# Kernel tuning notes

Hardware: AMD Instinct MI355X
Metric: run time of the kernel (lower is better)

The kernel has to match this reference:

```python
import jax, jax.numpy as jnp
import numpy as np
import math

N_QUBITS = 8
N_LAYERS = 3
BATCH = 8192
INPUT_DIM = 512


def _apply_1q(st, U, wire, batched):
    # st: (batch, 2,...,2) with N_QUBITS qubit axes; U: (2,2) or (batch,2,2)
    st = jnp.moveaxis(st, wire + 1, 1)
    sh = st.shape
    flat = st.reshape(sh[0], 2, -1)
    if batched:
        flat = jnp.einsum('bij,bjk->bik', U, flat)
    else:
        flat = jnp.einsum('ij,bjk->bik', U, flat)
    return jnp.moveaxis(flat.reshape(sh), 1, wire + 1)


def _apply_cnot(st, c, t):
    cax, tax = c + 1, t + 1
    zero = jnp.take(st, 0, axis=cax)
    one = jnp.take(st, 1, axis=cax)
    tax2 = tax - 1 if tax > cax else tax  # target axis shifts after control removed
    one = jnp.flip(one, axis=tax2)
    return jnp.stack([zero, one], axis=cax)


def _ry_batched(theta):
    # theta: (batch,) -> (batch,2,2) complex64
    c = jnp.cos(theta / 2)
    s = jnp.sin(theta / 2)
    row0 = jnp.stack([c, -s], axis=-1)
    row1 = jnp.stack([s, c], axis=-1)
    return jnp.stack([row0, row1], axis=-2).astype(jnp.complex64)


def _rot(phi, theta, omega):
    # PennyLane Rot = RZ(omega) RY(theta) RZ(phi), scalar params -> (2,2) complex64
    c = jnp.cos(theta / 2)
    s = jnp.sin(theta / 2)
    u00 = jnp.exp(-0.5j * (phi + omega)) * c
    u01 = -jnp.exp(0.5j * (phi - omega)) * s
    u10 = jnp.exp(-0.5j * (phi - omega)) * s
    u11 = jnp.exp(0.5j * (phi + omega)) * c
    return jnp.stack([jnp.stack([u00, u01]), jnp.stack([u10, u11])]).astype(jnp.complex64)


def _quantum_circuit(angles, q_weights):
    batch = angles.shape[0]
    st = jnp.zeros((batch, 2 ** N_QUBITS), jnp.complex64).at[:, 0].set(1.0)
    st = st.reshape((batch,) + (2,) * N_QUBITS)
    # AngleEmbedding with RY rotations
    for w in range(N_QUBITS):
        st = _apply_1q(st, _ry_batched(angles[:, w]), w, batched=True)
    # StronglyEntanglingLayers: Rot on each wire, then CNOT ring with range r
    for l in range(N_LAYERS):
        for w in range(N_QUBITS):
            st = _apply_1q(st, _rot(q_weights[l, w, 0], q_weights[l, w, 1], q_weights[l, w, 2]), w, batched=False)
        r = (l % (N_QUBITS - 1)) + 1
        for w in range(N_QUBITS):
            st = _apply_cnot(st, w, (w + r) % N_QUBITS)
    probs = st.real ** 2 + st.imag ** 2
    zs = []
    for w in range(N_QUBITS):
        p = jnp.moveaxis(probs, w + 1, 1).reshape(batch, 2, -1).sum(-1)
        zs.append(p[:, 0] - p[:, 1])  # <Z_w> = P(0) - P(1)
    return jnp.stack(zs, axis=-1)


def setup_inputs() -> dict:
    key = jax.random.key(0)
    k1, k2, k3 = jax.random.split(key, 3)
    x = jax.random.normal(k1, (BATCH, INPUT_DIM), dtype=jnp.float32)
    W = jax.random.normal(k2, (N_QUBITS, INPUT_DIM), dtype=jnp.float32) * (1.0 / math.sqrt(INPUT_DIM))
    b = jnp.zeros((N_QUBITS,), jnp.float32)
    scale = jnp.ones((N_QUBITS,), jnp.float32)
    bias = jnp.zeros((N_QUBITS,), jnp.float32)
    q_weights = 0.01 * jax.random.normal(k3, (N_LAYERS, N_QUBITS, 3), dtype=jnp.float32)
    return {"x": x, "W": W, "b": b, "scale": scale, "bias": bias, "q_weights": q_weights}


def reference(x, W, b, scale, bias, q_weights):
    proj = x @ W.T + b                                   # (batch, n_qubits)
    angles = jax.nn.sigmoid(proj * scale + bias) * jnp.float32(math.pi)
    return _quantum_circuit(angles, q_weights)           # (batch, n_qubits)
```

## Files before the change

### kernel.cpp

```cpp
#include <hip/hip_runtime.h>
#include <math.h>


namespace {

constexpr float PI_F = 3.14159265358979323846f;

struct Cx { float re, im; };

__device__ __forceinline__ float shfx(float v, int m) {
  return __shfl_xor(v, m, 64);
}

__device__ __forceinline__ void mix2(Cx &a, Cx &b,
    float u00r, float u00i, float u01r, float u01i,
    float u10r, float u10i, float u11r, float u11i) {
  float ar = a.re, ai = a.im, br = b.re, bi = b.im;
  a.re = u00r*ar - u00i*ai + u01r*br - u01i*bi;
  a.im = u00r*ai + u00i*ar + u01r*bi + u01i*br;
  b.re = u10r*ar - u10i*ai + u11r*br - u11i*bi;
  b.im = u10r*ai + u10i*ar + u11r*bi + u11i*br;
}

template<int W>
__device__ __forceinline__ void apply1q(Cx s[16],
    float u00r, float u00i, float u01r, float u01i,
    float u10r, float u10i, float u11r, float u11i, int lane) {
  if constexpr (W >= 4) {
    constexpr int step = 1 << (7 - W);
#pragma unroll
    for (int k = 0; k < 16; ++k)
      if (!(k & step))
        mix2(s[k], s[k + step], u00r,u00i,u01r,u01i,u10r,u10i,u11r,u11i);
  } else {
    constexpr int lm = 1 << (3 - W);
    const bool hi = (lane & lm) != 0;
    float cAr = hi ? u11r : u00r, cAi = hi ? u11i : u00i;
    float cBr = hi ? u10r : u01r, cBi = hi ? u10i : u01i;
#pragma unroll
    for (int k = 0; k < 16; ++k) {
      float tr = shfx(s[k].re, lm), ti = shfx(s[k].im, lm);
      float mr = s[k].re, mi = s[k].im;
      s[k].re = cAr*mr - cAi*mi + cBr*tr - cBi*ti;
      s[k].im = cAr*mi + cAi*mr + cBr*ti + cBi*tr;
    }
  }
}

template<int W>
__device__ __forceinline__ void ryW(Cx s[16], float ang, int lane) {
  float h = 0.5f * ang;
  float c = __cosf(h), sn = __sinf(h);
  apply1q<W>(s, c, 0.f, -sn, 0.f, sn, 0.f, c, 0.f, lane);
}

template<int L, int W>
__device__ __forceinline__ void rotW(Cx s[16], const float* __restrict__ qw, int lane) {
  float phi = qw[L*24 + W*3 + 0];
  float th  = qw[L*24 + W*3 + 1];
  float om  = qw[L*24 + W*3 + 2];
  float c  = __cosf(0.5f*th), sn = __sinf(0.5f*th);
  float a  = 0.5f*(phi + om), d = 0.5f*(phi - om);
  float ca = __cosf(a), sa = __sinf(a);
  float cd = __cosf(d), sd = __sinf(d);
  apply1q<W>(s, c*ca, -c*sa, -sn*cd, -sn*sd, sn*cd, -sn*sd, c*ca, c*sa, lane);
}

__device__ __forceinline__ void swapc(Cx &a, Cx &b) { Cx t = a; a = b; b = t; }

__device__ __forceinline__ void cswap(Cx &a, Cx &b, bool c) {
  float ar = a.re, ai = a.im;
  a.re = c ? b.re : a.re;  a.im = c ? b.im : a.im;
  b.re = c ? ar : b.re;    b.im = c ? ai : b.im;
}

template<int CW, int TW>
__device__ __forceinline__ void cnot(Cx s[16], int lane) {
  constexpr int pc = 7 - CW, pt = 7 - TW;
  if constexpr (pc >= 4 && pt >= 4) {
    constexpr int lmC = 1 << (pc - 4), lmT = 1 << (pt - 4);
    const bool ctl = (lane & lmC) != 0;
#pragma unroll
    for (int k = 0; k < 16; ++k) {
      float tr = shfx(s[k].re, lmT), ti = shfx(s[k].im, lmT);
      s[k].re = ctl ? tr : s[k].re;
      s[k].im = ctl ? ti : s[k].im;
    }
  } else if constexpr (pc >= 4) {
    constexpr int lmC = 1 << (pc - 4), step = 1 << pt;
    const bool ctl = (lane & lmC) != 0;
#pragma unroll
    for (int k = 0; k < 16; ++k)
      if (!(k & step)) cswap(s[k], s[k + step], ctl);
  } else if constexpr (pt >= 4) {
    constexpr int lmT = 1 << (pt - 4), cb = 1 << pc;
#pragma unroll
    for (int k = 0; k < 16; ++k)
      if (k & cb) {
        s[k].re = shfx(s[k].re, lmT);
        s[k].im = shfx(s[k].im, lmT);
      }
  } else {
    constexpr int cb = 1 << pc, tb = 1 << pt;
#pragma unroll
    for (int k = 0; k < 16; ++k)
      if ((k & cb) && !(k & tb)) swapc(s[k], s[k + tb]);
  }
}

template<int L>
__device__ __forceinline__ void rotLayer(Cx s[16], const float* __restrict__ qw, int lane) {
  rotW<L,0>(s, qw, lane); rotW<L,1>(s, qw, lane);
  rotW<L,2>(s, qw, lane); rotW<L,3>(s, qw, lane);
  rotW<L,4>(s, qw, lane); rotW<L,5>(s, qw, lane);
  rotW<L,6>(s, qw, lane); rotW<L,7>(s, qw, lane);
}

__global__ __launch_bounds__(256) void quantum_layer_kernel(
    const float* __restrict__ x, const float* __restrict__ Wm,
    const float* __restrict__ bvec, const float* __restrict__ scale,
    const float* __restrict__ bias, const float* __restrict__ qw,
    float* __restrict__ out) {
  const int tid  = threadIdx.x;
  const int lane = tid & 63;
  const int ll   = lane & 15;
  const int b    = blockIdx.x * 16 + (tid >> 4);

  const float4* x4 = (const float4*)(x + (size_t)b * 512);
  float4 xs[8];
#pragma unroll
  for (int j = 0; j < 8; ++j) xs[j] = x4[j * 16 + ll];
  const float4* W4 = (const float4*)Wm;
  float ang[8];
#pragma unroll
  for (int q = 0; q < 8; ++q) {
    float acc = 0.f;
#pragma unroll
    for (int j = 0; j < 8; ++j) {
      float4 w = W4[q * 128 + j * 16 + ll];
      acc += xs[j].x*w.x + xs[j].y*w.y + xs[j].z*w.z + xs[j].w*w.w;
    }
    ang[q] = acc;
  }
#pragma unroll
  for (int off = 8; off >= 1; off >>= 1)
#pragma unroll
    for (int q = 0; q < 8; ++q)
      ang[q] += shfx(ang[q], off);
#pragma unroll
  for (int q = 0; q < 8; ++q) {
    float t = (ang[q] + bvec[q]) * scale[q] + bias[q];
    ang[q] = PI_F / (1.f + __expf(-t));
  }

  Cx s[16];
#pragma unroll
  for (int k = 0; k < 16; ++k) { s[k].re = 0.f; s[k].im = 0.f; }
  s[0].re = (ll == 0) ? 1.f : 0.f;

  ryW<0>(s, ang[0], lane); ryW<1>(s, ang[1], lane);
  ryW<2>(s, ang[2], lane); ryW<3>(s, ang[3], lane);
  ryW<4>(s, ang[4], lane); ryW<5>(s, ang[5], lane);
  ryW<6>(s, ang[6], lane); ryW<7>(s, ang[7], lane);

  rotLayer<0>(s, qw, lane);
  cnot<0,1>(s, lane); cnot<1,2>(s, lane); cnot<2,3>(s, lane); cnot<3,4>(s, lane);
  cnot<4,5>(s, lane); cnot<5,6>(s, lane); cnot<6,7>(s, lane); cnot<7,0>(s, lane);

  rotLayer<1>(s, qw, lane);
  cnot<0,2>(s, lane); cnot<1,3>(s, lane); cnot<2,4>(s, lane); cnot<3,5>(s, lane);
  cnot<4,6>(s, lane); cnot<5,7>(s, lane); cnot<6,0>(s, lane); cnot<7,1>(s, lane);

  rotLayer<2>(s, qw, lane);
  cnot<0,3>(s, lane); cnot<1,4>(s, lane); cnot<2,5>(s, lane); cnot<3,6>(s, lane);
  cnot<4,7>(s, lane); cnot<5,0>(s, lane); cnot<6,1>(s, lane); cnot<7,2>(s, lane);

  float p[16];
#pragma unroll
  for (int k = 0; k < 16; ++k) p[k] = s[k].re*s[k].re + s[k].im*s[k].im;

  float q0[8], z7 = 0.f;
#pragma unroll
  for (int m = 0; m < 8; ++m) {
    q0[m] = p[2*m] + p[2*m+1];
    z7 += p[2*m] - p[2*m+1];
  }
  float q1[4], z6 = 0.f;
#pragma unroll
  for (int m = 0; m < 4; ++m) {
    q1[m] = q0[2*m] + q0[2*m+1];
    z6 += q0[2*m] - q0[2*m+1];
  }
  float q2a = q1[0] + q1[1], q2b = q1[2] + q1[3];
  float z5  = (q1[0] - q1[1]) + (q1[2] - q1[3]);
  float tot = q2a + q2b;
  float z4  = q2a - q2b;

  float z[8];
#pragma unroll
  for (int w = 0; w < 4; ++w)
    z[w] = ((ll >> (3 - w)) & 1) ? -tot : tot;
  z[4] = z4; z[5] = z5; z[6] = z6; z[7] = z7;

#pragma unroll
  for (int off = 8; off >= 1; off >>= 1)
#pragma unroll
    for (int w = 0; w < 8; ++w)
      z[w] += shfx(z[w], off);

  if (ll == 0) {
    float4* op = (float4*)(out + (size_t)b * 8);
    op[0] = make_float4(z[0], z[1], z[2], z[3]);
    op[1] = make_float4(z[4], z[5], z[6], z[7]);
  }
}

}

extern "C" void kernel_launch(void* const* d_in, const int* in_sizes, int n_in,
                              void* d_out, int out_size, void* d_ws, size_t ws_size,
                              hipStream_t stream) {
  const float* x     = (const float*)d_in[0];
  const float* Wm    = (const float*)d_in[1];
  const float* bvec  = (const float*)d_in[2];
  const float* scale = (const float*)d_in[3];
  const float* bias  = (const float*)d_in[4];
  const float* qw    = (const float*)d_in[5];
  float* out = (float*)d_out;

  constexpr int BATCH = 8192;
  dim3 grid(BATCH / 16), block(256);
  hipLaunchKernelGGL(quantum_layer_kernel, grid, block, 0, stream,
                     x, Wm, bvec, scale, bias, qw, out);
}
```

Measured before the change: 100.3 us.

## Build post-layer-0 state analytically and fold final CNOT ring into measurement

Replaces the RY embedding, first Rot layer and first CNOT ring with a closed-form product state. Each amplitude is computed as a product of per-wire fused 2-vectors, indexed through the permutation that the CNOT ring applies. The last CNOT ring is dropped, and its permutation is folded into the Z-expectation parity reduction through lane-dependent sign selection. This removes many shuffles and gate applications. It relies on intricate index algebra specific to the fixed ring ranges, so a mistake in the mapping would produce wrong outputs.

```diff
diff --git a/kernel.cpp b/kernel.cpp
--- a/kernel.cpp
+++ b/kernel.cpp
@@ -10,6 +10,20 @@
 
 __device__ __forceinline__ float shfx(float v, int m) {
   return __shfl_xor(v, m, 64);
+}
+
+__device__ __forceinline__ Cx cmul(Cx a, Cx b) {
+  Cx r;
+  r.re = a.re * b.re - a.im * b.im;
+  r.im = a.re * b.im + a.im * b.re;
+  return r;
+}
+
+__device__ __forceinline__ Cx csel(Cx lo, Cx hi, int c) {
+  Cx r;
+  r.re = c ? hi.re : lo.re;
+  r.im = c ? hi.im : lo.im;
+  return r;
 }
 
 __device__ __forceinline__ void mix2(Cx &a, Cx &b,
@@ -45,13 +59,6 @@
       s[k].im = cAr*mi + cAi*mr + cBr*ti + cBi*tr;
     }
   }
-}
-
-template<int W>
-__device__ __forceinline__ void ryW(Cx s[16], float ang, int lane) {
-  float h = 0.5f * ang;
-  float c = __cosf(h), sn = __sinf(h);
-  apply1q<W>(s, c, 0.f, -sn, 0.f, sn, 0.f, c, 0.f, lane);
 }
 
 template<int L, int W>
@@ -153,54 +160,99 @@
     ang[q] = PI_F / (1.f + __expf(-t));
   }
 
+  Cx v[8][2];
+#pragma unroll
+  for (int w = 0; w < 8; ++w) {
+    float h  = 0.5f * ang[w];
+    float c0 = __cosf(h), s0 = __sinf(h);
+    float phi = qw[w*3 + 0], th = qw[w*3 + 1], om = qw[w*3 + 2];
+    float cth = __cosf(0.5f*th), sth = __sinf(0.5f*th);
+    float a  = 0.5f*(phi + om), d = 0.5f*(phi - om);
+    float ca = __cosf(a), sa = __sinf(a);
+    float cd = __cosf(d), sd = __sinf(d);
+    v[w][0].re =  cth*ca*c0 - sth*cd*s0;
+    v[w][0].im = -cth*sa*c0 - sth*sd*s0;
+    v[w][1].re =  sth*cd*c0 + cth*ca*s0;
+    v[w][1].im = -sth*sd*c0 + cth*sa*s0;
+  }
+
+  const int b0 = ll & 1, b1 = (ll >> 1) & 1, b2 = (ll >> 2) & 1, b3 = (ll >> 3) & 1;
+
+  Cx A[2];
+  A[0] = cmul(csel(v[0][0], v[0][1], b3),     csel(v[1][0], v[1][1], b3 ^ b2));
+  A[1] = cmul(csel(v[0][0], v[0][1], b3 ^ 1), csel(v[1][0], v[1][1], b3 ^ b2 ^ 1));
+  Cx Lf = cmul(csel(v[2][0], v[2][1], b1 ^ b2), csel(v[3][0], v[3][1], b0 ^ b1));
+  Cx AL[2] = { cmul(A[0], Lf), cmul(A[1], Lf) };
+  Cx B[2];
+  B[0] = csel(v[4][0], v[4][1], b0);
+  B[1] = csel(v[4][0], v[4][1], b0 ^ 1);
+
+  Cx G01[2][2], G23[2][2];
+#pragma unroll
+  for (int t0 = 0; t0 < 2; ++t0)
+#pragma unroll
+    for (int t1 = 0; t1 < 2; ++t1)
+      G01[t0][t1] = cmul(AL[t0], v[7][t0 ^ t1]);
+#pragma unroll
+  for (int t2 = 0; t2 < 2; ++t2)
+#pragma unroll
+    for (int t3 = 0; t3 < 2; ++t3)
+      G23[t2][t3] = cmul(B[t3], v[5][t2 ^ t3]);
+
   Cx s[16];
 #pragma unroll
-  for (int k = 0; k < 16; ++k) { s[k].re = 0.f; s[k].im = 0.f; }
-  s[0].re = (ll == 0) ? 1.f : 0.f;
-
-  ryW<0>(s, ang[0], lane); ryW<1>(s, ang[1], lane);
-  ryW<2>(s, ang[2], lane); ryW<3>(s, ang[3], lane);
-  ryW<4>(s, ang[4], lane); ryW<5>(s, ang[5], lane);
-  ryW<6>(s, ang[6], lane); ryW<7>(s, ang[7], lane);
-
-  rotLayer<0>(s, qw, lane);
-  cnot<0,1>(s, lane); cnot<1,2>(s, lane); cnot<2,3>(s, lane); cnot<3,4>(s, lane);
-  cnot<4,5>(s, lane); cnot<5,6>(s, lane); cnot<6,7>(s, lane); cnot<7,0>(s, lane);
+  for (int k = 0; k < 16; ++k) {
+    const int kb0 = k & 1, kb1 = (k >> 1) & 1, kb2 = (k >> 2) & 1, kb3 = (k >> 3) & 1;
+    s[k] = cmul(cmul(G01[kb0][kb1], v[6][kb1 ^ kb2]), G23[kb2][kb3]);
+  }
 
   rotLayer<1>(s, qw, lane);
   cnot<0,2>(s, lane); cnot<1,3>(s, lane); cnot<2,4>(s, lane); cnot<3,5>(s, lane);
   cnot<4,6>(s, lane); cnot<5,7>(s, lane); cnot<6,0>(s, lane); cnot<7,1>(s, lane);
 
   rotLayer<2>(s, qw, lane);
-  cnot<0,3>(s, lane); cnot<1,4>(s, lane); cnot<2,5>(s, lane); cnot<3,6>(s, lane);
-  cnot<4,7>(s, lane); cnot<5,0>(s, lane); cnot<6,1>(s, lane); cnot<7,2>(s, lane);
 
   float p[16];
 #pragma unroll
   for (int k = 0; k < 16; ++k) p[k] = s[k].re*s[k].re + s[k].im*s[k].im;
 
-  float q0[8], z7 = 0.f;
+  float sA[8], dA[8];
 #pragma unroll
   for (int m = 0; m < 8; ++m) {
-    q0[m] = p[2*m] + p[2*m+1];
-    z7 += p[2*m] - p[2*m+1];
-  }
-  float q1[4], z6 = 0.f;
+    sA[m] = p[2*m] + p[2*m+1];
+    dA[m] = p[2*m] - p[2*m+1];
+  }
+  float sB[4], dB[4], nB[4];
 #pragma unroll
   for (int m = 0; m < 4; ++m) {
-    q1[m] = q0[2*m] + q0[2*m+1];
-    z6 += q0[2*m] - q0[2*m+1];
-  }
-  float q2a = q1[0] + q1[1], q2b = q1[2] + q1[3];
-  float z5  = (q1[0] - q1[1]) + (q1[2] - q1[3]);
-  float tot = q2a + q2b;
-  float z4  = q2a - q2b;
-
+    sB[m] = sA[2*m] + sA[2*m+1];
+    dB[m] = sA[2*m] - sA[2*m+1];
+    nB[m] = dA[2*m] + dA[2*m+1];
+  }
+  float sC[2], cC[2], tC[2], nC[2];
+#pragma unroll
+  for (int m = 0; m < 2; ++m) {
+    sC[m] = sB[2*m] + sB[2*m+1];
+    cC[m] = sB[2*m] - sB[2*m+1];
+    tC[m] = dB[2*m] + dB[2*m+1];
+    nC[m] = nB[2*m] + nB[2*m+1];
+  }
+  float R0 = sC[0] + sC[1];
+  float R8 = sC[0] - sC[1];
+  float R4 = cC[0] + cC[1];
+  float R2 = tC[0] + tC[1];
+  float R9 = nC[0] - nC[1];
+
+  const int g02 = b1 ^ b3, g1 = b0 ^ b2 ^ b3, g2 = b1 ^ b2, g36 = b0 ^ b3;
   float z[8];
-#pragma unroll
-  for (int w = 0; w < 4; ++w)
-    z[w] = ((ll >> (3 - w)) & 1) ? -tot : tot;
-  z[4] = z4; z[5] = z5; z[6] = z6; z[7] = z7;
+  z[0] = g02 ? -R4 : R4;
+  z[1] = g1  ? -R2 : R2;
+  z[2] = g2  ? -R9 : R9;
+  z[3] = g36 ? -R0 : R0;
+  z[4] = b2  ? -R8 : R8;
+  z[5] = b1  ? -R4 : R4;
+  z[6] = g36 ? -R2 : R2;
+  z[7] = b2  ? -R9 : R9;
 
 #pragma unroll
   for (int off = 8; off >= 1; off >>= 1)
```

After: 91.31 us. 9.0% less time.
